# Kernel tuning notes

Hardware: AMD Instinct MI355X
Metric: run time of the kernel (lower is better)

## Reference

```python
import jax, jax.numpy as jnp
import numpy as np

INPUT_SIZE = 512
HIDDEN_SIZE = 1024
OUTPUT_SIZE = 32
BATCH = 256
SEQ = 128


def setup_inputs() -> dict:
    key = jax.random.key(0)
    keys = jax.random.split(key, 20)
    stdv = 1.0 / np.sqrt(HIDDEN_SIZE)
    u = lambda k, shape: jax.random.uniform(k, shape, jnp.float32, -stdv, stdv)
    inp = {
        "inputs": jax.random.normal(keys[0], (BATCH, SEQ, INPUT_SIZE), jnp.float32),
        "w_ii": u(keys[1], (HIDDEN_SIZE, INPUT_SIZE)),
        "w_hi": u(keys[2], (HIDDEN_SIZE, HIDDEN_SIZE)),
        "b_ii": u(keys[3], (HIDDEN_SIZE,)),
        "b_hi": u(keys[4], (HIDDEN_SIZE,)),
        "w_if": u(keys[5], (HIDDEN_SIZE, INPUT_SIZE)),
        "w_hf": u(keys[6], (HIDDEN_SIZE, HIDDEN_SIZE)),
        "b_if": u(keys[7], (HIDDEN_SIZE,)),
        "b_hf": u(keys[8], (HIDDEN_SIZE,)),
        "w_io": u(keys[9], (HIDDEN_SIZE, INPUT_SIZE)),
        "w_ho": u(keys[10], (HIDDEN_SIZE, HIDDEN_SIZE)),
        "b_io": u(keys[11], (HIDDEN_SIZE,)),
        "b_ho": u(keys[12], (HIDDEN_SIZE,)),
        "w_ic": u(keys[13], (HIDDEN_SIZE, INPUT_SIZE)),
        "w_hc": u(keys[14], (HIDDEN_SIZE, HIDDEN_SIZE)),
        "b_ic": u(keys[15], (HIDDEN_SIZE,)),
        "b_hc": u(keys[16], (HIDDEN_SIZE,)),
        "w_fc": u(keys[17], (OUTPUT_SIZE, HIDDEN_SIZE)),
    }
    return inp


def reference(inputs, w_ii, w_hi, b_ii, b_hi, w_if, w_hf, b_if, b_hf,
              w_io, w_ho, b_io, b_ho, w_ic, w_hc, b_ic, b_hc, w_fc):
    # Deterministic eval path (train=False): plain hand-rolled LSTM over time,
    # last hidden -> fc -> log_softmax. Gates computed as in the torch code:
    # sigmoid(W_i* x + b_i* + W_h* h + b_h*), tanh for the cell candidate.
    B, T, I = inputs.shape
    H = w_ii.shape[0]

    def step(carry, x_t):  # x_t: [B, I]
        h, c = carry  # [B, H]
        i_g = jax.nn.sigmoid(x_t @ w_ii.T + b_ii + h @ w_hi.T + b_hi)
        f_g = jax.nn.sigmoid(x_t @ w_if.T + b_if + h @ w_hf.T + b_hf)
        g = jnp.tanh(x_t @ w_ic.T + b_ic + h @ w_hc.T + b_hc)
        o_g = jax.nn.sigmoid(x_t @ w_io.T + b_io + h @ w_ho.T + b_ho)
        c_n = f_g * c + i_g * g
        h_n = o_g * jnp.tanh(c_n)
        return (h_n, c_n), None

    h0 = jnp.zeros((B, H), inputs.dtype)
    c0 = jnp.zeros((B, H), inputs.dtype)
    (h_last, _), _ = jax.lax.scan(step, (h0, c0), jnp.swapaxes(inputs, 0, 1))
    logits = h_last @ w_fc.T  # [B, OUTPUT_SIZE]
    return jax.nn.log_softmax(logits, axis=1)
```

## Files before the change

kernel.cpp:

```cpp
#include <hip/hip_runtime.h>
#include <stdint.h>

#define GAS __attribute__((address_space(1)))
#define LAS __attribute__((address_space(3)))

typedef __bf16 v8bf __attribute__((ext_vector_type(8)));
typedef float v4f __attribute__((ext_vector_type(4)));
typedef unsigned short u16;
typedef unsigned long long u64;

constexpr int kB = 256, kT = 128, kI = 512, kH = 1024, kO = 32;
constexpr int kBlocks = 256, kThreads = 256;
constexpr int KSX = kI / 32;
constexpr int KSH = kH / 32;
constexpr int QX = KSX / 4;
constexpr int QH = KSH / 4;

constexpr size_t OFF_FLG = 0;
constexpr size_t OFF_H   = 8192;
constexpr size_t SZ_H    = (size_t)2 * kB * kH * 2;
constexpr size_t OFF_XT  = OFF_H + SZ_H;
constexpr size_t SZ_XT   = (size_t)kB * kT * kI * 2;
constexpr size_t OFF_WIT = OFF_XT + SZ_XT;
constexpr size_t SZ_WIT  = (size_t)kH * kI * 2;
constexpr size_t OFF_WHT = OFF_WIT + 4 * SZ_WIT;
constexpr size_t SZ_WHT  = (size_t)kH * kH * 2;

struct LstmParams {
  const u16* xt;
  const u16* wit[4];
  const u16* wht[4];
  const float* bi[4];
  const float* bh[4];
  const float* wfc;
  float* out;
  unsigned* flags;
  u16* hbuf;
};

static __device__ __forceinline__ float b2f(u16 v) {
  union { float f; uint32_t i; } u; u.i = ((uint32_t)v) << 16; return u.f;
}
static __device__ __forceinline__ u16 f2b(float f) {
  union { float f; uint32_t i; } u; u.f = f;
  return (u16)((u.i + 0x7fffu + ((u.i >> 16) & 1u)) >> 16);
}
static __device__ __forceinline__ float sigm(float x) { return 1.f / (1.f + __expf(-x)); }
static __device__ __forceinline__ float tanh_f(float x) {
  float e = __expf(2.f * x);
  return 1.f - 2.f / (e + 1.f);
}
static __device__ __forceinline__ void ld16c(const void* g, void* l) {
  __builtin_amdgcn_global_load_lds((const GAS uint32_t*)g, (LAS uint32_t*)l, 16, 0, 0x11);
}

__global__ __launch_bounds__(256) void cvt_x_tile(const float* __restrict__ x,
                                                  u16* __restrict__ xt) {
  const int gid = blockIdx.x * 256 + threadIdx.x;
  const int lane = gid & 63;
  const int ks = (gid >> 6) & 15;
  const int mi = (gid >> 10) & 3;
  const int mt = (gid >> 12) & 3;
  const int t  = gid >> 14;
  const int m = mt * 64 + mi * 16 + (lane & 15);
  const int k = ks * 32 + (lane >> 4) * 8;
  const float4* s = (const float4*)(x + ((size_t)m * kT + t) * kI + k);
  const float4 a = s[0], b = s[1];
  uint4 o = {f2b(a.x) | ((uint32_t)f2b(a.y) << 16), f2b(a.z) | ((uint32_t)f2b(a.w) << 16),
             f2b(b.x) | ((uint32_t)f2b(b.y) << 16), f2b(b.z) | ((uint32_t)f2b(b.w) << 16)};
  *(uint4*)(xt + (size_t)gid * 8) = o;
}

__global__ __launch_bounds__(256) void cvt_w_tile(const float* __restrict__ w,
                                                  u16* __restrict__ wt,
                                                  int K, int lgKS) {
  const int gid = blockIdx.x * 256 + threadIdx.x;
  const int lane = gid & 63;
  const int rest = gid >> 6;
  const int ks = rest & ((1 << lgKS) - 1);
  const int ut2 = rest >> lgKS;
  const int u = ut2 * 16 + (lane & 15);
  const int k = ks * 32 + (lane >> 4) * 8;
  const float4* s = (const float4*)(w + (size_t)u * K + k);
  const float4 a = s[0], b = s[1];
  uint4 o = {f2b(a.x) | ((uint32_t)f2b(a.y) << 16), f2b(a.z) | ((uint32_t)f2b(a.w) << 16),
             f2b(b.x) | ((uint32_t)f2b(b.y) << 16), f2b(b.z) | ((uint32_t)f2b(b.w) << 16)};
  *(uint4*)(wt + (size_t)gid * 8) = o;
}

__global__ __launch_bounds__(kThreads, 2) void lstm_kernel(LstmParams p) {
  __shared__ __align__(16) char smem[133120];
  v4f* Red = (v4f*)smem;
  u16* Hout = (u16*)(smem + 131072);
  u16* shFC = (u16*)smem;

  const int tid = threadIdx.x;
  const int lane = tid & 63;
  const int wv = tid >> 6;
  const int blk = blockIdx.x;
  const int mt = blk & 3;
  const int ut = blk >> 2;

  const int mloc = lane & 15;
  const int q = lane >> 4;
  const int uglob = ut * 16 + mloc;

  unsigned* gflags = p.flags + mt * 256;

  float bias[4];
#pragma unroll
  for (int g = 0; g < 4; ++g) bias[g] = p.bi[g][uglob] + p.bh[g][uglob];

  float creg[4] = {0.f, 0.f, 0.f, 0.f};

  v8bf bhh[QH][4];
#pragma unroll
  for (int g = 0; g < 4; ++g)
#pragma unroll
    for (int i = 0; i < QH; ++i)
      bhh[i][g] = *((const v8bf*)p.wht[g] + ((size_t)(ut * KSH + wv * QH + i) * 64 + lane));

  for (int t = 0; t < kT; ++t) {
    v4f acc[4][4];
#pragma unroll
    for (int m = 0; m < 4; ++m)
#pragma unroll
      for (int g = 0; g < 4; ++g) acc[m][g] = (v4f){0.f, 0.f, 0.f, 0.f};

    const v8bf* xf = (const v8bf*)p.xt + ((size_t)(t * 4 + mt) * 4 * KSX) * 64;
#pragma unroll
    for (int i = 0; i < QX; ++i) {
      v8bf bxl[4];
#pragma unroll
      for (int g = 0; g < 4; ++g)
        bxl[g] = *((const v8bf*)p.wit[g] + ((size_t)(ut * KSX + wv * QX + i) * 64 + lane));
#pragma unroll
      for (int mi = 0; mi < 4; ++mi) {
        const v8bf a = xf[(size_t)(mi * KSX + wv * QX + i) * 64 + lane];
#pragma unroll
        for (int g = 0; g < 4; ++g)
          acc[mi][g] = __builtin_amdgcn_mfma_f32_16x16x32_bf16(a, bxl[g], acc[mi][g], 0, 0, 0);
      }
    }

    if (t > 0) {
      if (wv == 0) {
        while (true) {
          unsigned v = __hip_atomic_load(&gflags[lane * 4], __ATOMIC_RELAXED,
                                         __HIP_MEMORY_SCOPE_AGENT);
          if (__ballot(v >= (unsigned)t) == ~0ull) break;
          __builtin_amdgcn_s_sleep(1);
        }
      }
      __syncthreads();

      const char* hread = (const char*)(p.hbuf + (size_t)(t & 1) * kB * kH);
      char* myHs = smem + wv * 32768;
#pragma unroll
      for (int mi = 0; mi < 4; ++mi)
#pragma unroll
        for (int i = 0; i < QH; ++i) {
          const size_t sl = (size_t)((mt * 4 + mi) * KSH + wv * QH + i);
          ld16c(hread + sl * 1024 + lane * 16, myHs + (mi * QH + i) * 1024);
        }

      __syncthreads();

#pragma unroll
      for (int mi = 0; mi < 4; ++mi)
#pragma unroll
        for (int i = 0; i < QH; ++i) {
          const v8bf a = *(const v8bf*)(myHs + (mi * QH + i) * 1024 + lane * 16);
#pragma unroll
          for (int g = 0; g < 4; ++g)
            acc[mi][g] = __builtin_amdgcn_mfma_f32_16x16x32_bf16(a, bhh[i][g], acc[mi][g], 0, 0, 0);
        }
    }

    __syncthreads();

#pragma unroll
    for (int m = 0; m < 4; ++m)
#pragma unroll
      for (int g = 0; g < 4; ++g)
        Red[(wv * 16 + g * 4 + m) * 64 + lane] = acc[m][g];
    __syncthreads();

    v4f gacc[4];
#pragma unroll
    for (int g = 0; g < 4; ++g) {
      v4f s = Red[(0 * 16 + g * 4 + wv) * 64 + lane];
#pragma unroll
      for (int wvp = 1; wvp < 4; ++wvp) {
        const v4f z = Red[(wvp * 16 + g * 4 + wv) * 64 + lane];
#pragma unroll
        for (int r = 0; r < 4; ++r) s[r] += z[r];
      }
      gacc[g] = s;
    }

#pragma unroll
    for (int r = 0; r < 4; ++r) {
      const float iv = sigm(gacc[0][r] + bias[0]);
      const float fv = sigm(gacc[1][r] + bias[1]);
      const float gv = tanh_f(gacc[2][r] + bias[2]);
      const float ov = sigm(gacc[3][r] + bias[3]);
      creg[r] = fv * creg[r] + iv * gv;
      const float hv = ov * tanh_f(creg[r]);
      Hout[(wv * 16 + q * 4 + r) * 16 + mloc] = f2b(hv);
    }
    __syncthreads();

    {
      u16* hw = p.hbuf + (size_t)((t + 1) & 1) * kB * kH;
      const int c = tid >> 5;
      const int mi_s = c >> 1;
      const int hbit = c & 1;
      const int hi = (ut * 2 + hbit) & 3;
      const int row16 = (tid & 31) >> 1;
      const int j0 = (tid & 1) * 4;
      const u64 v = *(const u64*)&Hout[(mi_s * 16 + row16) * 16 + hbit * 8 + j0];
      u64* dst = (u64*)((char*)hw + ((size_t)((mt * 4 + mi_s) * KSH + (ut >> 1)) * 1024)
                        + hi * 256 + row16 * 16 + j0 * 2);
      __hip_atomic_store(dst, v, __ATOMIC_RELAXED, __HIP_MEMORY_SCOPE_AGENT);
    }

    __syncthreads();
    if (tid == 0)
      __hip_atomic_fetch_add(&gflags[ut * 4], 1u, __ATOMIC_RELAXED,
                             __HIP_MEMORY_SCOPE_AGENT);
  }

  if (blk < 32) {
    const int gg = blk >> 3;
    if (wv == 0) {
      while (true) {
        unsigned v = __hip_atomic_load(&p.flags[gg * 256 + lane * 4], __ATOMIC_RELAXED,
                                       __HIP_MEMORY_SCOPE_AGENT);
        if (__ballot(v >= (unsigned)kT) == ~0ull) break;
        __builtin_amdgcn_s_sleep(1);
      }
    }
    __syncthreads();
    {
      const int mi = (blk >> 1) & 3;
      const int ks2 = tid >> 3;
      const int ug = (tid >> 1) & 3;
      const int rh = tid & 1;
      u64* hf = (u64*)p.hbuf;
#pragma unroll
      for (int rr = 0; rr < 4; ++rr) {
        const int row_l = rh * 4 + rr;
        const int r16 = (blk & 1) * 8 + row_l;
        const int L = r16 | (ug << 4);
        const size_t fi = ((size_t)((gg * 4 + mi) * KSH + ks2) * 64 + L) * 2;
        const u64 a = __hip_atomic_load(hf + fi, __ATOMIC_RELAXED, __HIP_MEMORY_SCOPE_AGENT);
        const u64 b = __hip_atomic_load(hf + fi + 1, __ATOMIC_RELAXED, __HIP_MEMORY_SCOPE_AGENT);
        u64* d = (u64*)&shFC[row_l * kH + ks2 * 32 + ug * 8];
        d[0] = a; d[1] = b;
      }
    }
    __syncthreads();
    const int row = tid >> 5;
    const int col = tid & 31;
    const u16* hr = &shFC[row * kH];
    const float* wr = p.wfc + (size_t)col * kH;
    float s = 0.f;
    for (int k = 0; k < kH; k += 4) {
      const float4 w4 = *(const float4*)(wr + k);
      s += b2f(hr[k]) * w4.x + b2f(hr[k + 1]) * w4.y +
           b2f(hr[k + 2]) * w4.z + b2f(hr[k + 3]) * w4.w;
    }
    float mx = s;
#pragma unroll
    for (int off = 16; off; off >>= 1) mx = fmaxf(mx, __shfl_xor(mx, off, 32));
    const float ex = __expf(s - mx);
    float se = ex;
#pragma unroll
    for (int off = 16; off; off >>= 1) se += __shfl_xor(se, off, 32);
    p.out[(blk * 8 + row) * kO + col] = s - mx - __logf(se);
  }
}

extern "C" void kernel_launch(void* const* d_in, const int* in_sizes, int n_in,
                              void* d_out, int out_size, void* d_ws, size_t ws_size,
                              hipStream_t stream) {
  (void)in_sizes; (void)n_in; (void)out_size; (void)ws_size;
  char* ws = (char*)d_ws;

  u16* xt = (u16*)(ws + OFF_XT);
  u16 *wit[4], *wht[4];
  for (int g = 0; g < 4; ++g) {
    wit[g] = (u16*)(ws + OFF_WIT + (size_t)g * SZ_WIT);
    wht[g] = (u16*)(ws + OFF_WHT + (size_t)g * SZ_WHT);
  }

  const int gsrc[4] = {1, 5, 13, 9};

  hipMemsetAsync(d_ws, 0, 8192, stream);

  cvt_x_tile<<<8192, 256, 0, stream>>>((const float*)d_in[0], xt);
  for (int g = 0; g < 4; ++g) {
    cvt_w_tile<<<256, 256, 0, stream>>>((const float*)d_in[gsrc[g]], wit[g], kI, 4);
    cvt_w_tile<<<512, 256, 0, stream>>>((const float*)d_in[gsrc[g] + 1], wht[g], kH, 5);
  }

  LstmParams p;
  p.xt = xt;
  for (int g = 0; g < 4; ++g) {
    p.wit[g] = wit[g];
    p.wht[g] = wht[g];
    p.bi[g] = (const float*)d_in[gsrc[g] + 2];
    p.bh[g] = (const float*)d_in[gsrc[g] + 3];
  }
  p.wfc = (const float*)d_in[17];
  p.out = (float*)d_out;
  p.flags = (unsigned*)(ws + OFF_FLG);
  p.hbuf = (u16*)(ws + OFF_H);

  void* args[] = {&p};
  hipError_t e = hipLaunchCooperativeKernel((void*)lstm_kernel, dim3(kBlocks),
                                            dim3(kThreads), args, 0, stream);
  if (e != hipSuccess) {
    (void)hipGetLastError();
    lstm_kernel<<<dim3(kBlocks), dim3(kThreads), 0, stream>>>(p);
  }
}
```

Before: 1.487 ms.

## Rotate per-timestep hidden buffers, load h directly to registers, aggregate flag counters

Stores each timestep's hidden state in its own workspace slot when the workspace is large enough. This removes the double-buffer write-after-read hazard and lets h be loaded straight from global memory into registers instead of staging it through LDS with an extra barrier. The per-block readiness flags become four aggregated counters polled with a longer sleep, which cuts polling traffic but adds atomic contention on the shared counters. The rotation path needs about 129 hidden-state buffers of workspace and falls back to the old scheme otherwise.

```diff
diff --git a/kernel.cpp b/kernel.cpp
--- a/kernel.cpp
+++ b/kernel.cpp
@@ -16,15 +16,17 @@
 constexpr int QX = KSX / 4;
 constexpr int QH = KSH / 4;
 
-constexpr size_t OFF_FLG = 0;
-constexpr size_t OFF_H   = 8192;
-constexpr size_t SZ_H    = (size_t)2 * kB * kH * 2;
-constexpr size_t OFF_XT  = OFF_H + SZ_H;
-constexpr size_t SZ_XT   = (size_t)kB * kT * kI * 2;
-constexpr size_t OFF_WIT = OFF_XT + SZ_XT;
-constexpr size_t SZ_WIT  = (size_t)kH * kI * 2;
-constexpr size_t OFF_WHT = OFF_WIT + 4 * SZ_WIT;
-constexpr size_t SZ_WHT  = (size_t)kH * kH * 2;
+constexpr size_t OFF_FLG  = 0;
+constexpr size_t OFF_XT   = 8192;
+constexpr size_t SZ_XT    = (size_t)kB * kT * kI * 2;
+constexpr size_t OFF_WIT  = OFF_XT + SZ_XT;
+constexpr size_t SZ_WIT   = (size_t)kH * kI * 2;
+constexpr size_t OFF_WHT  = OFF_WIT + 4 * SZ_WIT;
+constexpr size_t SZ_WHT   = (size_t)kH * kH * 2;
+constexpr size_t OFF_H    = OFF_WHT + 4 * SZ_WHT;
+constexpr size_t SZ_H1    = (size_t)kB * kH * 2;
+constexpr size_t NEED_ROT = OFF_H + (size_t)(kT + 1) * SZ_H1;
+constexpr size_t NEED_MIN = OFF_H + 2 * SZ_H1;
 
 struct LstmParams {
   const u16* xt;
@@ -36,6 +38,7 @@
   float* out;
   unsigned* flags;
   u16* hbuf;
+  int rot;
 };
 
 static __device__ __forceinline__ float b2f(u16 v) {
@@ -145,36 +148,55 @@
 
     if (t > 0) {
       if (wv == 0) {
+        const unsigned need = 16u * (unsigned)t;
+        unsigned* sc = &gflags[(lane & 3) * 64];
         while (true) {
-          unsigned v = __hip_atomic_load(&gflags[lane * 4], __ATOMIC_RELAXED,
-                                         __HIP_MEMORY_SCOPE_AGENT);
-          if (__ballot(v >= (unsigned)t) == ~0ull) break;
-          __builtin_amdgcn_s_sleep(1);
+          unsigned v = __hip_atomic_load(sc, __ATOMIC_RELAXED, __HIP_MEMORY_SCOPE_AGENT);
+          if (__ballot(v >= need) == ~0ull) break;
+          __builtin_amdgcn_s_sleep(4);
         }
       }
       __syncthreads();
 
-      const char* hread = (const char*)(p.hbuf + (size_t)(t & 1) * kB * kH);
-      char* myHs = smem + wv * 32768;
-#pragma unroll
-      for (int mi = 0; mi < 4; ++mi)
-#pragma unroll
-        for (int i = 0; i < QH; ++i) {
-          const size_t sl = (size_t)((mt * 4 + mi) * KSH + wv * QH + i);
-          ld16c(hread + sl * 1024 + lane * 16, myHs + (mi * QH + i) * 1024);
+      if (p.rot) {
+        const v8bf* hf = (const v8bf*)(p.hbuf + (size_t)t * (size_t)(kB * kH));
+#pragma unroll
+        for (int mi = 0; mi < 4; ++mi) {
+          v8bf av[QH];
+#pragma unroll
+          for (int i = 0; i < QH; ++i)
+            av[i] = hf[(size_t)((mt * 4 + mi) * KSH + wv * QH + i) * 64 + lane];
+#pragma unroll
+          for (int i = 0; i < QH; ++i)
+#pragma unroll
+            for (int g = 0; g < 4; ++g)
+              acc[mi][g] = __builtin_amdgcn_mfma_f32_16x16x32_bf16(av[i], bhh[i][g],
+                                                                   acc[mi][g], 0, 0, 0);
         }
-
-      __syncthreads();
-
-#pragma unroll
-      for (int mi = 0; mi < 4; ++mi)
-#pragma unroll
-        for (int i = 0; i < QH; ++i) {
-          const v8bf a = *(const v8bf*)(myHs + (mi * QH + i) * 1024 + lane * 16);
-#pragma unroll
-          for (int g = 0; g < 4; ++g)
-            acc[mi][g] = __builtin_amdgcn_mfma_f32_16x16x32_bf16(a, bhh[i][g], acc[mi][g], 0, 0, 0);
-        }
+      } else {
+        const char* hread = (const char*)(p.hbuf + (size_t)(t & 1) * kB * kH);
+        char* myHs = smem + wv * 32768;
+#pragma unroll
+        for (int mi = 0; mi < 4; ++mi)
+#pragma unroll
+          for (int i = 0; i < QH; ++i) {
+            const size_t sl = (size_t)((mt * 4 + mi) * KSH + wv * QH + i);
+            ld16c(hread + sl * 1024 + lane * 16, myHs + (mi * QH + i) * 1024);
+          }
+
+        __syncthreads();
+
+#pragma unroll
+        for (int mi = 0; mi < 4; ++mi)
+#pragma unroll
+          for (int i = 0; i < QH; ++i) {
+            const v8bf a = *(const v8bf*)(myHs + (mi * QH + i) * 1024 + lane * 16);
+#pragma unroll
+            for (int g = 0; g < 4; ++g)
+              acc[mi][g] = __builtin_amdgcn_mfma_f32_16x16x32_bf16(a, bhh[i][g],
+                                                                   acc[mi][g], 0, 0, 0);
+          }
+      }
     }
 
     __syncthreads();
@@ -212,7 +234,7 @@
     __syncthreads();
 
     {
-      u16* hw = p.hbuf + (size_t)((t + 1) & 1) * kB * kH;
+      u16* hw = p.hbuf + (size_t)(p.rot ? (t + 1) : ((t + 1) & 1)) * (size_t)(kB * kH);
       const int c = tid >> 5;
       const int mi_s = c >> 1;
       const int hbit = c & 1;
@@ -227,18 +249,19 @@
 
     __syncthreads();
     if (tid == 0)
-      __hip_atomic_fetch_add(&gflags[ut * 4], 1u, __ATOMIC_RELAXED,
+      __hip_atomic_fetch_add(&gflags[(ut & 3) * 64], 1u, __ATOMIC_RELAXED,
                              __HIP_MEMORY_SCOPE_AGENT);
   }
 
   if (blk < 32) {
     const int gg = blk >> 3;
     if (wv == 0) {
+      const unsigned need = 16u * (unsigned)kT;
+      unsigned* sc = &p.flags[gg * 256 + (lane & 3) * 64];
       while (true) {
-        unsigned v = __hip_atomic_load(&p.flags[gg * 256 + lane * 4], __ATOMIC_RELAXED,
-                                       __HIP_MEMORY_SCOPE_AGENT);
-        if (__ballot(v >= (unsigned)kT) == ~0ull) break;
-        __builtin_amdgcn_s_sleep(1);
+        unsigned v = __hip_atomic_load(sc, __ATOMIC_RELAXED, __HIP_MEMORY_SCOPE_AGENT);
+        if (__ballot(v >= need) == ~0ull) break;
+        __builtin_amdgcn_s_sleep(4);
       }
     }
     __syncthreads();
@@ -247,7 +270,7 @@
       const int ks2 = tid >> 3;
       const int ug = (tid >> 1) & 3;
       const int rh = tid & 1;
-      u64* hf = (u64*)p.hbuf;
+      u64* hf = (u64*)(p.hbuf + (size_t)(p.rot ? kT : 0) * (size_t)(kB * kH));
 #pragma unroll
       for (int rr = 0; rr < 4; ++rr) {
         const int row_l = rh * 4 + rr;
@@ -285,7 +308,7 @@
 extern "C" void kernel_launch(void* const* d_in, const int* in_sizes, int n_in,
                               void* d_out, int out_size, void* d_ws, size_t ws_size,
                               hipStream_t stream) {
-  (void)in_sizes; (void)n_in; (void)out_size; (void)ws_size;
+  (void)in_sizes; (void)n_in; (void)out_size;
   char* ws = (char*)d_ws;
 
   u16* xt = (u16*)(ws + OFF_XT);
@@ -317,6 +340,7 @@
   p.out = (float*)d_out;
   p.flags = (unsigned*)(ws + OFF_FLG);
   p.hbuf = (u16*)(ws + OFF_H);
+  p.rot = (ws_size >= NEED_ROT) ? 1 : 0;
 
   void* args[] = {&p};
   hipError_t e = hipLaunchCooperativeKernel((void*)lstm_kernel, dim3(kBlocks),
```

Measured after the change: 2.480 ms. +66.7%, slower.

## Halve LSTM block count with 8-wave blocks sharing staged h tiles

Applied to the files above, without the earlier changes.

Restructures the persistent LSTM kernel from 256 blocks of 4 waves to 128 blocks of 8 waves. Each block now owns 32 hidden units, with two wave halves sharing each staged h slice in LDS, so h traffic from global memory is halved. The h staging is split between wave halves and overlapped with MFMA using explicit waitcnt and sched barriers. This cuts the number of blocks in the grid-wide flag barrier per step. The cost is more work per block, larger shared memory, and a 512-thread block whose register pressure under launch_bounds(512,2) may force spills.

```diff
diff --git a/kernel.cpp b/kernel.cpp
--- a/kernel.cpp
+++ b/kernel.cpp
@@ -10,7 +10,7 @@
 typedef unsigned long long u64;
 
 constexpr int kB = 256, kT = 128, kI = 512, kH = 1024, kO = 32;
-constexpr int kBlocks = 256, kThreads = 256;
+constexpr int kBlocks = 128, kThreads = 512;
 constexpr int KSX = kI / 32;
 constexpr int KSH = kH / 32;
 constexpr int QX = KSX / 4;
@@ -89,7 +89,7 @@
 }
 
 __global__ __launch_bounds__(kThreads, 2) void lstm_kernel(LstmParams p) {
-  __shared__ __align__(16) char smem[133120];
+  __shared__ __align__(16) char smem[135168];
   v4f* Red = (v4f*)smem;
   u16* Hout = (u16*)(smem + 131072);
   u16* shFC = (u16*)smem;
@@ -97,13 +97,16 @@
   const int tid = threadIdx.x;
   const int lane = tid & 63;
   const int wv = tid >> 6;
+  const int kq = wv >> 1;
+  const int uh = wv & 1;
   const int blk = blockIdx.x;
   const int mt = blk & 3;
-  const int ut = blk >> 2;
+  const int us = blk >> 2;
+  const int utl = us * 2 + uh;
 
   const int mloc = lane & 15;
   const int q = lane >> 4;
-  const int uglob = ut * 16 + mloc;
+  const int uglob = us * 32 + uh * 16 + mloc;
 
   unsigned* gflags = p.flags + mt * 256;
 
@@ -118,7 +121,7 @@
   for (int g = 0; g < 4; ++g)
 #pragma unroll
     for (int i = 0; i < QH; ++i)
-      bhh[i][g] = *((const v8bf*)p.wht[g] + ((size_t)(ut * KSH + wv * QH + i) * 64 + lane));
+      bhh[i][g] = *((const v8bf*)p.wht[g] + ((size_t)(utl * KSH + kq * QH + i) * 64 + lane));
 
   for (int t = 0; t < kT; ++t) {
     v4f acc[4][4];
@@ -133,10 +136,10 @@
       v8bf bxl[4];
 #pragma unroll
       for (int g = 0; g < 4; ++g)
-        bxl[g] = *((const v8bf*)p.wit[g] + ((size_t)(ut * KSX + wv * QX + i) * 64 + lane));
+        bxl[g] = *((const v8bf*)p.wit[g] + ((size_t)(utl * KSX + kq * QX + i) * 64 + lane));
 #pragma unroll
       for (int mi = 0; mi < 4; ++mi) {
-        const v8bf a = xf[(size_t)(mi * KSX + wv * QX + i) * 64 + lane];
+        const v8bf a = xf[(size_t)(mi * KSX + kq * QX + i) * 64 + lane];
 #pragma unroll
         for (int g = 0; g < 4; ++g)
           acc[mi][g] = __builtin_amdgcn_mfma_f32_16x16x32_bf16(a, bxl[g], acc[mi][g], 0, 0, 0);
@@ -146,7 +149,7 @@
     if (t > 0) {
       if (wv == 0) {
         while (true) {
-          unsigned v = __hip_atomic_load(&gflags[lane * 4], __ATOMIC_RELAXED,
+          unsigned v = __hip_atomic_load(&gflags[(lane & 31) * 4], __ATOMIC_RELAXED,
                                          __HIP_MEMORY_SCOPE_AGENT);
           if (__ballot(v >= (unsigned)t) == ~0ull) break;
           __builtin_amdgcn_s_sleep(1);
@@ -155,26 +158,50 @@
       __syncthreads();
 
       const char* hread = (const char*)(p.hbuf + (size_t)(t & 1) * kB * kH);
-      char* myHs = smem + wv * 32768;
-#pragma unroll
-      for (int mi = 0; mi < 4; ++mi)
-#pragma unroll
-        for (int i = 0; i < QH; ++i) {
-          const size_t sl = (size_t)((mt * 4 + mi) * KSH + wv * QH + i);
-          ld16c(hread + sl * 1024 + lane * 16, myHs + (mi * QH + i) * 1024);
-        }
-
+      char* kqs = smem + kq * 32768;
+
+#define STAGE_MI(MI)                                                          \
+  _Pragma("unroll")                                                           \
+  for (int i = 0; i < QH; ++i) {                                              \
+    const size_t sl = (size_t)((mt * 4 + (MI)) * KSH + kq * QH + i);          \
+    ld16c(hread + sl * 1024 + lane * 16, kqs + ((MI) * QH + i) * 1024);       \
+  }
+#define COMPUTE_MI(MI)                                                        \
+  _Pragma("unroll")                                                           \
+  for (int i = 0; i < QH; ++i) {                                              \
+    const v8bf a = *(const v8bf*)(kqs + ((MI) * QH + i) * 1024 + lane * 16);  \
+    _Pragma("unroll")                                                         \
+    for (int g = 0; g < 4; ++g)                                               \
+      acc[(MI)][g] =                                                          \
+          __builtin_amdgcn_mfma_f32_16x16x32_bf16(a, bhh[i][g], acc[(MI)][g], \
+                                                  0, 0, 0);                   \
+  }
+
+      if (uh == 0) {
+        STAGE_MI(0) STAGE_MI(1)
+        asm volatile("s_waitcnt vmcnt(8)" ::: "memory");
+        __builtin_amdgcn_sched_barrier(0);
+        COMPUTE_MI(0)
+        asm volatile("s_waitcnt vmcnt(0)" ::: "memory");
+        __builtin_amdgcn_sched_barrier(0);
+        COMPUTE_MI(1)
+      } else {
+        STAGE_MI(2) STAGE_MI(3)
+        asm volatile("s_waitcnt vmcnt(8)" ::: "memory");
+        __builtin_amdgcn_sched_barrier(0);
+        COMPUTE_MI(2)
+        asm volatile("s_waitcnt vmcnt(0)" ::: "memory");
+        __builtin_amdgcn_sched_barrier(0);
+        COMPUTE_MI(3)
+      }
       __syncthreads();
-
-#pragma unroll
-      for (int mi = 0; mi < 4; ++mi)
-#pragma unroll
-        for (int i = 0; i < QH; ++i) {
-          const v8bf a = *(const v8bf*)(myHs + (mi * QH + i) * 1024 + lane * 16);
-#pragma unroll
-          for (int g = 0; g < 4; ++g)
-            acc[mi][g] = __builtin_amdgcn_mfma_f32_16x16x32_bf16(a, bhh[i][g], acc[mi][g], 0, 0, 0);
-        }
+      if (uh == 0) {
+        COMPUTE_MI(2) COMPUTE_MI(3)
+      } else {
+        COMPUTE_MI(0) COMPUTE_MI(1)
+      }
+#undef STAGE_MI
+#undef COMPUTE_MI
     }
 
     __syncthreads();
@@ -183,16 +210,16 @@
     for (int m = 0; m < 4; ++m)
 #pragma unroll
       for (int g = 0; g < 4; ++g)
-        Red[(wv * 16 + g * 4 + m) * 64 + lane] = acc[m][g];
+        Red[((uh * 4 + kq) * 16 + g * 4 + m) * 64 + lane] = acc[m][g];
     __syncthreads();
 
     v4f gacc[4];
 #pragma unroll
     for (int g = 0; g < 4; ++g) {
-      v4f s = Red[(0 * 16 + g * 4 + wv) * 64 + lane];
-#pragma unroll
-      for (int wvp = 1; wvp < 4; ++wvp) {
-        const v4f z = Red[(wvp * 16 + g * 4 + wv) * 64 + lane];
+      v4f s = Red[((uh * 4 + 0) * 16 + g * 4 + kq) * 64 + lane];
+#pragma unroll
+      for (int kqp = 1; kqp < 4; ++kqp) {
+        const v4f z = Red[((uh * 4 + kqp) * 16 + g * 4 + kq) * 64 + lane];
 #pragma unroll
         for (int r = 0; r < 4; ++r) s[r] += z[r];
       }
@@ -207,27 +234,27 @@
       const float ov = sigm(gacc[3][r] + bias[3]);
       creg[r] = fv * creg[r] + iv * gv;
       const float hv = ov * tanh_f(creg[r]);
-      Hout[(wv * 16 + q * 4 + r) * 16 + mloc] = f2b(hv);
+      Hout[(kq * 16 + q * 4 + r) * 32 + uh * 16 + mloc] = f2b(hv);
     }
     __syncthreads();
 
     {
       u16* hw = p.hbuf + (size_t)((t + 1) & 1) * kB * kH;
-      const int c = tid >> 5;
-      const int mi_s = c >> 1;
-      const int hbit = c & 1;
-      const int hi = (ut * 2 + hbit) & 3;
-      const int row16 = (tid & 31) >> 1;
-      const int j0 = (tid & 1) * 4;
-      const u64 v = *(const u64*)&Hout[(mi_s * 16 + row16) * 16 + hbit * 8 + j0];
-      u64* dst = (u64*)((char*)hw + ((size_t)((mt * 4 + mi_s) * KSH + (ut >> 1)) * 1024)
-                        + hi * 256 + row16 * 16 + j0 * 2);
+      const int mi_s = tid >> 7;
+      const int idx = tid & 127;
+      const int L = idx >> 1;
+      const int j0 = (idx & 1) * 4;
+      const int row16 = L & 15;
+      const int kg = L >> 4;
+      const u64 v = *(const u64*)&Hout[(mi_s * 16 + row16) * 32 + kg * 8 + j0];
+      u64* dst = (u64*)((char*)hw + ((size_t)((mt * 4 + mi_s) * KSH + us) * 1024)
+                        + kg * 256 + row16 * 16 + j0 * 2);
       __hip_atomic_store(dst, v, __ATOMIC_RELAXED, __HIP_MEMORY_SCOPE_AGENT);
     }
 
     __syncthreads();
     if (tid == 0)
-      __hip_atomic_fetch_add(&gflags[ut * 4], 1u, __ATOMIC_RELAXED,
+      __hip_atomic_fetch_add(&gflags[us * 4], 1u, __ATOMIC_RELAXED,
                              __HIP_MEMORY_SCOPE_AGENT);
   }
 
@@ -235,14 +262,14 @@
     const int gg = blk >> 3;
     if (wv == 0) {
       while (true) {
-        unsigned v = __hip_atomic_load(&p.flags[gg * 256 + lane * 4], __ATOMIC_RELAXED,
-                                       __HIP_MEMORY_SCOPE_AGENT);
+        unsigned v = __hip_atomic_load(&p.flags[gg * 256 + (lane & 31) * 4],
+                                       __ATOMIC_RELAXED, __HIP_MEMORY_SCOPE_AGENT);
         if (__ballot(v >= (unsigned)kT) == ~0ull) break;
         __builtin_amdgcn_s_sleep(1);
       }
     }
     __syncthreads();
-    {
+    if (tid < 256) {
       const int mi = (blk >> 1) & 3;
       const int ks2 = tid >> 3;
       const int ug = (tid >> 1) & 3;
@@ -261,24 +288,26 @@
       }
     }
     __syncthreads();
-    const int row = tid >> 5;
-    const int col = tid & 31;
-    const u16* hr = &shFC[row * kH];
-    const float* wr = p.wfc + (size_t)col * kH;
-    float s = 0.f;
-    for (int k = 0; k < kH; k += 4) {
-      const float4 w4 = *(const float4*)(wr + k);
-      s += b2f(hr[k]) * w4.x + b2f(hr[k + 1]) * w4.y +
-           b2f(hr[k + 2]) * w4.z + b2f(hr[k + 3]) * w4.w;
-    }
-    float mx = s;
-#pragma unroll
-    for (int off = 16; off; off >>= 1) mx = fmaxf(mx, __shfl_xor(mx, off, 32));
-    const float ex = __expf(s - mx);
-    float se = ex;
-#pragma unroll
-    for (int off = 16; off; off >>= 1) se += __shfl_xor(se, off, 32);
-    p.out[(blk * 8 + row) * kO + col] = s - mx - __logf(se);
+    if (tid < 256) {
+      const int row = tid >> 5;
+      const int col = tid & 31;
+      const u16* hr = &shFC[row * kH];
+      const float* wr = p.wfc + (size_t)col * kH;
+      float s = 0.f;
+      for (int k = 0; k < kH; k += 4) {
+        const float4 w4 = *(const float4*)(wr + k);
+        s += b2f(hr[k]) * w4.x + b2f(hr[k + 1]) * w4.y +
+             b2f(hr[k + 2]) * w4.z + b2f(hr[k + 3]) * w4.w;
+      }
+      float mx = s;
+#pragma unroll
+      for (int off = 16; off; off >>= 1) mx = fmaxf(mx, __shfl_xor(mx, off, 32));
+      const float ex = __expf(s - mx);
+      float se = ex;
+#pragma unroll
+      for (int off = 16; off; off >>= 1) se += __shfl_xor(se, off, 32);
+      p.out[(blk * 8 + row) * kO + col] = s - mx - __logf(se);
+    }
   }
 }
 
```

Measured after the change: 1.857 ms. 1.25x slower.

## Split batch tiles across twice as many blocks and pipeline h staging

Applied to the files above, without the earlier changes.

Doubles the persistent grid from 256 to 512 blocks, with each block now handling two 16-row batch sub-tiles instead of four. This halves per-block shared memory so more blocks fit per CU. The h-staging loads are split into two halves with explicit vmcnt waits, so MFMA on the first half overlaps the second half's loads. The reduction and write-back are reworked for the smaller tile. In exchange, the recurrent weights are duplicated in registers across twice as many blocks, and the per-step flag barrier now has eight groups, adding synchronisation traffic.

```diff
diff --git a/kernel.cpp b/kernel.cpp
--- a/kernel.cpp
+++ b/kernel.cpp
@@ -10,7 +10,7 @@
 typedef unsigned long long u64;
 
 constexpr int kB = 256, kT = 128, kI = 512, kH = 1024, kO = 32;
-constexpr int kBlocks = 256, kThreads = 256;
+constexpr int kBlocks = 512, kThreads = 256;
 constexpr int KSX = kI / 32;
 constexpr int KSH = kH / 32;
 constexpr int QX = KSX / 4;
@@ -89,29 +89,32 @@
 }
 
 __global__ __launch_bounds__(kThreads, 2) void lstm_kernel(LstmParams p) {
-  __shared__ __align__(16) char smem[133120];
+  __shared__ __align__(16) char smem[66560];
   v4f* Red = (v4f*)smem;
-  u16* Hout = (u16*)(smem + 131072);
+  float* Redf = (float*)smem;
+  u16* Hout = (u16*)(smem + 65536);
   u16* shFC = (u16*)smem;
 
   const int tid = threadIdx.x;
   const int lane = tid & 63;
   const int wv = tid >> 6;
   const int blk = blockIdx.x;
-  const int mt = blk & 3;
-  const int ut = blk >> 2;
+  const int mt8 = blk >> 6;
+  const int ut = blk & 63;
+  const int mt4 = mt8 >> 1;
+  const int mib = (mt8 & 1) * 2;
 
   const int mloc = lane & 15;
   const int q = lane >> 4;
   const int uglob = ut * 16 + mloc;
 
-  unsigned* gflags = p.flags + mt * 256;
+  unsigned* gflags = p.flags + mt8 * 256;
 
   float bias[4];
 #pragma unroll
   for (int g = 0; g < 4; ++g) bias[g] = p.bi[g][uglob] + p.bh[g][uglob];
 
-  float creg[4] = {0.f, 0.f, 0.f, 0.f};
+  float creg[2] = {0.f, 0.f};
 
   v8bf bhh[QH][4];
 #pragma unroll
@@ -121,13 +124,13 @@
       bhh[i][g] = *((const v8bf*)p.wht[g] + ((size_t)(ut * KSH + wv * QH + i) * 64 + lane));
 
   for (int t = 0; t < kT; ++t) {
-    v4f acc[4][4];
-#pragma unroll
-    for (int m = 0; m < 4; ++m)
+    v4f acc[2][4];
+#pragma unroll
+    for (int m = 0; m < 2; ++m)
 #pragma unroll
       for (int g = 0; g < 4; ++g) acc[m][g] = (v4f){0.f, 0.f, 0.f, 0.f};
 
-    const v8bf* xf = (const v8bf*)p.xt + ((size_t)(t * 4 + mt) * 4 * KSX) * 64;
+    const v8bf* xf = (const v8bf*)p.xt + ((size_t)(t * 4 + mt4) * 4 * KSX) * 64;
 #pragma unroll
     for (int i = 0; i < QX; ++i) {
       v8bf bxl[4];
@@ -135,11 +138,11 @@
       for (int g = 0; g < 4; ++g)
         bxl[g] = *((const v8bf*)p.wit[g] + ((size_t)(ut * KSX + wv * QX + i) * 64 + lane));
 #pragma unroll
-      for (int mi = 0; mi < 4; ++mi) {
-        const v8bf a = xf[(size_t)(mi * KSX + wv * QX + i) * 64 + lane];
+      for (int ml = 0; ml < 2; ++ml) {
+        const v8bf a = xf[(size_t)((mib + ml) * KSX + wv * QX + i) * 64 + lane];
 #pragma unroll
         for (int g = 0; g < 4; ++g)
-          acc[mi][g] = __builtin_amdgcn_mfma_f32_16x16x32_bf16(a, bxl[g], acc[mi][g], 0, 0, 0);
+          acc[ml][g] = __builtin_amdgcn_mfma_f32_16x16x32_bf16(a, bxl[g], acc[ml][g], 0, 0, 0);
       }
     }
 
@@ -155,73 +158,83 @@
       __syncthreads();
 
       const char* hread = (const char*)(p.hbuf + (size_t)(t & 1) * kB * kH);
-      char* myHs = smem + wv * 32768;
-#pragma unroll
-      for (int mi = 0; mi < 4; ++mi)
-#pragma unroll
-        for (int i = 0; i < QH; ++i) {
-          const size_t sl = (size_t)((mt * 4 + mi) * KSH + wv * QH + i);
-          ld16c(hread + sl * 1024 + lane * 16, myHs + (mi * QH + i) * 1024);
-        }
-
-      __syncthreads();
-
-#pragma unroll
-      for (int mi = 0; mi < 4; ++mi)
-#pragma unroll
-        for (int i = 0; i < QH; ++i) {
-          const v8bf a = *(const v8bf*)(myHs + (mi * QH + i) * 1024 + lane * 16);
-#pragma unroll
-          for (int g = 0; g < 4; ++g)
-            acc[mi][g] = __builtin_amdgcn_mfma_f32_16x16x32_bf16(a, bhh[i][g], acc[mi][g], 0, 0, 0);
-        }
-    }
-
-    __syncthreads();
-
-#pragma unroll
-    for (int m = 0; m < 4; ++m)
+      char* myHs = smem + wv * 16384;
+
+#define STAGE_ML(ML)                                                          \
+  _Pragma("unroll")                                                           \
+  for (int i = 0; i < QH; ++i) {                                              \
+    const size_t sl = (size_t)((mt4 * 4 + mib + (ML)) * KSH + wv * QH + i);   \
+    ld16c(hread + sl * 1024 + lane * 16, myHs + ((ML) * QH + i) * 1024);      \
+  }
+#define COMPUTE_ML(ML)                                                        \
+  _Pragma("unroll")                                                           \
+  for (int i = 0; i < QH; ++i) {                                              \
+    const v8bf a = *(const v8bf*)(myHs + ((ML) * QH + i) * 1024 + lane * 16); \
+    _Pragma("unroll")                                                         \
+    for (int g = 0; g < 4; ++g)                                               \
+      acc[(ML)][g] = __builtin_amdgcn_mfma_f32_16x16x32_bf16(                 \
+          a, bhh[i][g], acc[(ML)][g], 0, 0, 0);                               \
+  }
+
+      STAGE_ML(0) STAGE_ML(1)
+      asm volatile("s_waitcnt vmcnt(8)" ::: "memory");
+      __builtin_amdgcn_sched_barrier(0);
+      COMPUTE_ML(0)
+      asm volatile("s_waitcnt vmcnt(0)" ::: "memory");
+      __builtin_amdgcn_sched_barrier(0);
+      COMPUTE_ML(1)
+#undef STAGE_ML
+#undef COMPUTE_ML
+    }
+
+    __syncthreads();
+
+#pragma unroll
+    for (int ml = 0; ml < 2; ++ml)
 #pragma unroll
       for (int g = 0; g < 4; ++g)
-        Red[(wv * 16 + g * 4 + m) * 64 + lane] = acc[m][g];
-    __syncthreads();
-
-    v4f gacc[4];
-#pragma unroll
-    for (int g = 0; g < 4; ++g) {
-      v4f s = Red[(0 * 16 + g * 4 + wv) * 64 + lane];
-#pragma unroll
-      for (int wvp = 1; wvp < 4; ++wvp) {
-        const v4f z = Red[(wvp * 16 + g * 4 + wv) * 64 + lane];
-#pragma unroll
-        for (int r = 0; r < 4; ++r) s[r] += z[r];
-      }
-      gacc[g] = s;
-    }
-
-#pragma unroll
-    for (int r = 0; r < 4; ++r) {
-      const float iv = sigm(gacc[0][r] + bias[0]);
-      const float fv = sigm(gacc[1][r] + bias[1]);
-      const float gv = tanh_f(gacc[2][r] + bias[2]);
-      const float ov = sigm(gacc[3][r] + bias[3]);
+        Red[(wv * 8 + ml * 4 + g) * 64 + lane] = acc[ml][g];
+    __syncthreads();
+
+#pragma unroll
+    for (int r = 0; r < 2; ++r) {
+      const int lrow = wv * 8 + q * 2 + r;
+      const int ml = lrow >> 4;
+      const int r16 = lrow & 15;
+      const int qp = r16 >> 2;
+      const int reg = r16 & 3;
+      float gacc[4];
+#pragma unroll
+      for (int g = 0; g < 4; ++g) {
+        float s = 0.f;
+#pragma unroll
+        for (int kq = 0; kq < 4; ++kq)
+          s += Redf[((kq * 8 + ml * 4 + g) * 64 + qp * 16 + mloc) * 4 + reg];
+        gacc[g] = s;
+      }
+      const float iv = sigm(gacc[0] + bias[0]);
+      const float fv = sigm(gacc[1] + bias[1]);
+      const float gv = tanh_f(gacc[2] + bias[2]);
+      const float ov = sigm(gacc[3] + bias[3]);
       creg[r] = fv * creg[r] + iv * gv;
       const float hv = ov * tanh_f(creg[r]);
-      Hout[(wv * 16 + q * 4 + r) * 16 + mloc] = f2b(hv);
-    }
-    __syncthreads();
-
-    {
+      Hout[lrow * 16 + mloc] = f2b(hv);
+    }
+    __syncthreads();
+
+    if (tid < 128) {
       u16* hw = p.hbuf + (size_t)((t + 1) & 1) * kB * kH;
-      const int c = tid >> 5;
-      const int mi_s = c >> 1;
-      const int hbit = c & 1;
-      const int hi = (ut * 2 + hbit) & 3;
-      const int row16 = (tid & 31) >> 1;
-      const int j0 = (tid & 1) * 4;
-      const u64 v = *(const u64*)&Hout[(mi_s * 16 + row16) * 16 + hbit * 8 + j0];
-      u64* dst = (u64*)((char*)hw + ((size_t)((mt * 4 + mi_s) * KSH + (ut >> 1)) * 1024)
-                        + hi * 256 + row16 * 16 + j0 * 2);
+      const int run = tid >> 5;
+      const int ml = run >> 1;
+      const int hbit = run & 1;
+      const int idx = tid & 31;
+      const int row16 = idx >> 1;
+      const int j0 = (idx & 1) * 4;
+      const int hi = (ut & 1) * 2 + hbit;
+      const u64 v = *(const u64*)&Hout[(ml * 16 + row16) * 16 + hbit * 8 + j0];
+      u64* dst = (u64*)((char*)hw +
+                        ((size_t)((mt4 * 4 + mib + ml) * KSH + (ut >> 1)) * 1024) +
+                        hi * 256 + row16 * 16 + j0 * 2);
       __hip_atomic_store(dst, v, __ATOMIC_RELAXED, __HIP_MEMORY_SCOPE_AGENT);
     }
 
@@ -232,10 +245,10 @@
   }
 
   if (blk < 32) {
-    const int gg = blk >> 3;
+    const int gg8 = blk >> 2;
     if (wv == 0) {
       while (true) {
-        unsigned v = __hip_atomic_load(&p.flags[gg * 256 + lane * 4], __ATOMIC_RELAXED,
+        unsigned v = __hip_atomic_load(&p.flags[gg8 * 256 + lane * 4], __ATOMIC_RELAXED,
                                        __HIP_MEMORY_SCOPE_AGENT);
         if (__ballot(v >= (unsigned)kT) == ~0ull) break;
         __builtin_amdgcn_s_sleep(1);
@@ -243,6 +256,7 @@
     }
     __syncthreads();
     {
+      const int gg4 = blk >> 3;
       const int mi = (blk >> 1) & 3;
       const int ks2 = tid >> 3;
       const int ug = (tid >> 1) & 3;
@@ -253,7 +267,7 @@
         const int row_l = rh * 4 + rr;
         const int r16 = (blk & 1) * 8 + row_l;
         const int L = r16 | (ug << 4);
-        const size_t fi = ((size_t)((gg * 4 + mi) * KSH + ks2) * 64 + L) * 2;
+        const size_t fi = ((size_t)((gg4 * 4 + mi) * KSH + ks2) * 64 + L) * 2;
         const u64 a = __hip_atomic_load(hf + fi, __ATOMIC_RELAXED, __HIP_MEMORY_SCOPE_AGENT);
         const u64 b = __hip_atomic_load(hf + fi + 1, __ATOMIC_RELAXED, __HIP_MEMORY_SCOPE_AGENT);
         u64* d = (u64*)&shFC[row_l * kH + ks2 * 32 + ug * 8];
```

After: 1.216 ms. 1.22x faster.
